# Performance work log

Measured on AMD Instinct MI355X. Metric: run time of the kernel, lower is better.

The kernel has to match this reference:

```python
import jax, jax.numpy as jnp
import numpy as np

BN_EPS = 1e-5


def _fps(xyz, n_centers):
    """Furthest point sampling. xyz: (B,N,3) -> idx (B,n_centers) int32.
    Deterministic start at index 0 (torch version uses randint start)."""
    B, N, _ = xyz.shape
    batch_ar = jnp.arange(B)

    def step(carry, _):
        distances, farthest = carry  # (B,N), (B,)
        center = xyz[batch_ar, farthest]  # (B,3)
        d = jnp.sum((xyz - center[:, None, :]) ** 2, axis=-1)  # (B,N)
        distances = jnp.minimum(distances, d)
        new_far = jnp.argmax(distances, axis=-1)
        return (distances, new_far), farthest

    init = (jnp.full((B, N), jnp.inf, dtype=xyz.dtype),
            jnp.zeros((B,), dtype=jnp.int32))
    _, idxs = jax.lax.scan(step, init, None, length=n_centers)  # (n_centers, B)
    return idxs.T  # (B, n_centers)


def _knn_group(xyz, centers, k):
    """xyz:(B,N,3), centers:(B,M,3) -> patches (B,M,k,3) center-relative."""
    # (B,M,N) squared distances
    dists = jnp.sum((centers[:, :, None, :] - xyz[:, None, :, :]) ** 2, axis=-1)
    _, idx = jax.lax.top_k(-dists, k)  # (B,M,k) smallest distances
    # gather neighbor coords: (B,M,k,3)
    patches = jnp.take_along_axis(xyz[:, None, :, :], idx[..., None], axis=2)
    return patches - centers[:, :, None, :]


def _bn_eval(x, gamma, beta):
    # BatchNorm1d in eval mode: running_mean=0, running_var=1
    return x * (gamma / jnp.sqrt(1.0 + BN_EPS)) + beta


def _mini_pointnet(patches, W1, b1, g1, bt1, W2, b2, g2, bt2, W3, b3, g3, bt3):
    B, M, k, C = patches.shape
    x = patches.reshape(B * M * k, C)
    x = jax.nn.relu(_bn_eval(x @ W1 + b1, g1, bt1))
    x = jax.nn.relu(_bn_eval(x @ W2 + b2, g2, bt2))
    x = jax.nn.relu(_bn_eval(x @ W3 + b3, g3, bt3))
    x = x.reshape(B * M, k, -1).max(axis=1)
    return x.reshape(B, M, -1)


def setup_inputs() -> dict:
    key = jax.random.key(0)
    ks = jax.random.split(key, 8)
    B, N = 16, 16384
    embed = 256

    def lin(kk, fan_in, fan_out):
        bound = 1.0 / np.sqrt(fan_in)
        k1, k2 = jax.random.split(kk)
        W = jax.random.uniform(k1, (fan_in, fan_out), jnp.float32, -bound, bound)
        b = jax.random.uniform(k2, (fan_out,), jnp.float32, -bound, bound)
        return W, b

    W1, b1 = lin(ks[1], 3, 64)
    W2, b2 = lin(ks[2], 64, 128)
    W3, b3 = lin(ks[3], 128, embed)
    return {
        "xyz": jax.random.normal(ks[0], (B, N, 3), jnp.float32),
        "W1": W1, "b1": b1, "g1": jnp.ones((64,)), "bt1": jnp.zeros((64,)),
        "W2": W2, "b2": b2, "g2": jnp.ones((128,)), "bt2": jnp.zeros((128,)),
        "W3": W3, "b3": b3, "g3": jnp.ones((embed,)), "bt3": jnp.zeros((embed,)),
        "n_centers": 256,
        "k": 32,
    }


def reference(xyz, W1, b1, g1, bt1, W2, b2, g2, bt2, W3, b3, g3, bt3,
              n_centers, k):
    center_idx = _fps(xyz, n_centers)  # (B, M)
    centers = jnp.take_along_axis(xyz, center_idx[..., None], axis=1)  # (B,M,3)
    patches = _knn_group(xyz, centers, k)  # (B,M,k,3)
    tokens = _mini_pointnet(patches, W1, b1, g1, bt1, W2, b2, g2, bt2,
                            W3, b3, g3, bt3)
    return tokens, centers
```

## Files before the change

kernel.cpp:

```cpp
#include <hip/hip_runtime.h>

constexpr int B   = 16;
constexpr int N   = 16384;
constexpr int M   = 256;
constexpr int K   = 32;
constexpr int EMB = 256;

__device__ __forceinline__ float sqdist(float px, float py, float pz,
                                        float cx, float cy, float cz) {
  float dx = __fsub_rn(px, cx);
  float dy = __fsub_rn(py, cy);
  float dz = __fsub_rn(pz, cz);
  return __fadd_rn(__fadd_rn(__fmul_rn(dx, dx), __fmul_rn(dy, dy)),
                   __fmul_rn(dz, dz));
}

constexpr int FT = 512;
constexpr int FP = N / FT;
constexpr int FW = FT / 64;

__global__ __launch_bounds__(FT, 2) void fps_kernel(
    const float* __restrict__ xyz, float* __restrict__ centers) {
  const int b = blockIdx.x;
  const int tid = threadIdx.x;
  const float* base = xyz + (size_t)b * N * 3;

  float px[FP], py[FP], pz[FP], dist[FP];
#pragma unroll
  for (int j = 0; j < FP; ++j) {
    int n = tid + j * FT;
    px[j] = base[n * 3 + 0];
    py[j] = base[n * 3 + 1];
    pz[j] = base[n * 3 + 2];
    dist[j] = __builtin_inff();
  }

  __shared__ float s_pv[2][FW];
  __shared__ int s_pn[2][FW];

  float cx = base[0], cy = base[1], cz = base[2];

  for (int it = 0; it < M; ++it) {
    if (tid == 0) {
      float* co = centers + ((size_t)b * M + it) * 3;
      co[0] = cx; co[1] = cy; co[2] = cz;
    }
    const int p = it & 1;

    float bv = -1.0f;
    int bj = 0;
#pragma unroll
    for (int j = 0; j < FP; ++j) {
      float d = sqdist(px[j], py[j], pz[j], cx, cy, cz);
      float nd = fminf(dist[j], d);
      dist[j] = nd;
      bool g = nd > bv;
      bv = g ? nd : bv;
      bj = g ? j : bj;
    }
    int bn = bj * FT + tid;

#pragma unroll
    for (int mm = 32; mm >= 1; mm >>= 1) {
      float ov = __shfl_xor(bv, mm, 64);
      int on = __shfl_xor(bn, mm, 64);
      if (ov > bv || (ov == bv && on < bn)) { bv = ov; bn = on; }
    }
    if ((tid & 63) == 0) {
      s_pv[p][tid >> 6] = bv;
      s_pn[p][tid >> 6] = bn;
    }
    __syncthreads();

    float v = s_pv[p][0];
    int n = s_pn[p][0];
#pragma unroll
    for (int w = 1; w < FW; ++w) {
      float ov = s_pv[p][w];
      int on = s_pn[p][w];
      if (ov > v || (ov == v && on < n)) { v = ov; n = on; }
    }
    cx = base[(size_t)n * 3 + 0];
    cy = base[(size_t)n * 3 + 1];
    cz = base[(size_t)n * 3 + 2];
  }
}

constexpr int KT = 256;
constexpr int CAP = 512;
constexpr int NBUCKET = 1024;

__global__ __launch_bounds__(KT) void knn_kernel(
    const float* __restrict__ xyz, const float* __restrict__ centers,
    float* __restrict__ patches) {
  const int blk = blockIdx.x;
  const int b = blk >> 8;
  const int tid = threadIdx.x;
  const float* base = xyz + (size_t)b * N * 3;

  __shared__ int hist[NBUCKET];
  __shared__ unsigned cb[CAP];
  __shared__ int ci[CAP];
  __shared__ int s_nin, s_ncand, s_tb;
  __shared__ int s_wsum[KT / 64];
  __shared__ float s_cc[3];

  if (tid == 0) {
    const float* c = centers + (size_t)blk * 3;
    s_cc[0] = c[0]; s_cc[1] = c[1]; s_cc[2] = c[2];
    s_nin = 0; s_ncand = 0;
  }
  for (int i = tid; i < NBUCKET; i += KT) hist[i] = 0;
  __syncthreads();

  const float cx = s_cc[0], cy = s_cc[1], cz = s_cc[2];

  for (int n = tid; n < N; n += KT) {
    float d = sqdist(base[n * 3], base[n * 3 + 1], base[n * 3 + 2], cx, cy, cz);
    atomicAdd(&hist[__float_as_uint(d) >> 21], 1);
  }
  __syncthreads();

  int h0[4];
  int loc = 0;
#pragma unroll
  for (int i = 0; i < 4; ++i) { h0[i] = hist[tid * 4 + i]; loc += h0[i]; }
  int lane = tid & 63, wid = tid >> 6;
  int scan = loc;
  for (int off = 1; off < 64; off <<= 1) {
    int o = __shfl_up(scan, off, 64);
    if (lane >= off) scan += o;
  }
  if (lane == 63) s_wsum[wid] = scan;
  __syncthreads();
  int woff = 0;
  for (int w = 0; w < wid; ++w) woff += s_wsum[w];
  int c0 = woff + scan - loc;
#pragma unroll
  for (int i = 0; i < 4; ++i) {
    int c1 = c0 + h0[i];
    if (c0 < K && c1 >= K) s_tb = tid * 4 + i;
    c0 = c1;
  }
  __syncthreads();
  const int tb = s_tb;
  const unsigned lo = (unsigned)tb << 21;
  const unsigned hi = (unsigned)(tb + 1) << 21;

  for (int n = tid; n < N; n += KT) {
    float x = base[n * 3], y = base[n * 3 + 1], z = base[n * 3 + 2];
    float d = sqdist(x, y, z, cx, cy, cz);
    unsigned bits = __float_as_uint(d);
    if (bits < lo) {
      int pos = atomicAdd(&s_nin, 1);
      float* p = patches + ((size_t)blk * K + pos) * 3;
      p[0] = __fsub_rn(x, cx); p[1] = __fsub_rn(y, cy); p[2] = __fsub_rn(z, cz);
    } else if (bits < hi) {
      int q = atomicAdd(&s_ncand, 1);
      if (q < CAP) { cb[q] = bits; ci[q] = n; }
    }
  }
  __syncthreads();

  const int nin = s_nin;
  const int ncand = min(s_ncand, CAP);
  const int nsel = K - nin;
  for (int j = tid; j < ncand; j += KT) {
    unsigned bj = cb[j];
    int ij = ci[j];
    int rank = 0;
    for (int i2 = 0; i2 < ncand; ++i2) {
      unsigned bv = cb[i2];
      int iv = ci[i2];
      rank += (bv < bj || (bv == bj && iv < ij)) ? 1 : 0;
    }
    if (rank < nsel) {
      float x = base[ij * 3], y = base[ij * 3 + 1], z = base[ij * 3 + 2];
      float* p = patches + ((size_t)blk * K + nin + rank) * 3;
      p[0] = __fsub_rn(x, cx); p[1] = __fsub_rn(y, cy); p[2] = __fsub_rn(z, cz);
    }
  }
}

constexpr int MT = 128;

__global__ __launch_bounds__(MT) void mlp_kernel(
    const float* __restrict__ patches,
    const float* __restrict__ W1, const float* __restrict__ b1,
    const float* __restrict__ g1, const float* __restrict__ bt1,
    const float* __restrict__ W2, const float* __restrict__ b2,
    const float* __restrict__ g2, const float* __restrict__ bt2,
    const float* __restrict__ W3, const float* __restrict__ b3,
    const float* __restrict__ g3, const float* __restrict__ bt3,
    float* __restrict__ tokens) {
  const int pm = blockIdx.x;
  const int tid = threadIdx.x;
  __shared__ float xs[3][K];
  __shared__ float h1s[64 * K];
  __shared__ float h2s[128 * K];
  __shared__ float pms[2][EMB];

  const float* patch = patches + (size_t)pm * (K * 3);
  if (tid < 96) xs[tid % 3][tid / 3] = patch[tid];
  __syncthreads();

  const int cg = tid & 63;
  const int half = tid >> 6;
  const int pt0 = half * 16;
  const float rs = 1.0f / sqrtf(1.0f + 1e-5f);

  {
    const int c = cg;
    const float w0 = W1[c], w1 = W1[64 + c], w2 = W1[128 + c];
    const float bb = b1[c];
    const float sc = g1[c] * rs, be = bt1[c];
    float o[16];
#pragma unroll
    for (int p = 0; p < 16; ++p) {
      int pt = pt0 + p;
      float a = xs[0][pt] * w0 + xs[1][pt] * w1 + xs[2][pt] * w2 + bb;
      o[p] = fmaxf(a * sc + be, 0.0f);
    }
    const int so = (c & 7) << 2;
#pragma unroll
    for (int p4 = 0; p4 < 16; p4 += 4) {
      *(float4*)&h1s[c * K + ((pt0 + p4) ^ so)] =
          make_float4(o[p4], o[p4 + 1], o[p4 + 2], o[p4 + 3]);
    }
  }
  __syncthreads();

  {
    const int c = cg * 2;
    float acc0[16], acc1[16];
    const float bb0 = b2[c], bb1 = b2[c + 1];
#pragma unroll
    for (int p = 0; p < 16; ++p) { acc0[p] = bb0; acc1[p] = bb1; }
    for (int k = 0; k < 64; ++k) {
      const float2 w = *(const float2*)(W2 + k * 128 + c);
      const int so = (k & 7) << 2;
      float4 x0 = *(const float4*)&h1s[k * K + ((pt0 + 0) ^ so)];
      float4 x1 = *(const float4*)&h1s[k * K + ((pt0 + 4) ^ so)];
      float4 x2 = *(const float4*)&h1s[k * K + ((pt0 + 8) ^ so)];
      float4 x3 = *(const float4*)&h1s[k * K + ((pt0 + 12) ^ so)];
      float xv[16] = {x0.x, x0.y, x0.z, x0.w, x1.x, x1.y, x1.z, x1.w,
                      x2.x, x2.y, x2.z, x2.w, x3.x, x3.y, x3.z, x3.w};
#pragma unroll
      for (int p = 0; p < 16; ++p) {
        acc0[p] += xv[p] * w.x;
        acc1[p] += xv[p] * w.y;
      }
    }
    const float sc0 = g2[c] * rs, be0 = bt2[c];
    const float sc1 = g2[c + 1] * rs, be1 = bt2[c + 1];
    float o0[16], o1[16];
#pragma unroll
    for (int p = 0; p < 16; ++p) {
      o0[p] = fmaxf(acc0[p] * sc0 + be0, 0.0f);
      o1[p] = fmaxf(acc1[p] * sc1 + be1, 0.0f);
    }
    const int soa = (c & 7) << 2, sob = ((c + 1) & 7) << 2;
#pragma unroll
    for (int p4 = 0; p4 < 16; p4 += 4) {
      *(float4*)&h2s[c * K + ((pt0 + p4) ^ soa)] =
          make_float4(o0[p4], o0[p4 + 1], o0[p4 + 2], o0[p4 + 3]);
      *(float4*)&h2s[(c + 1) * K + ((pt0 + p4) ^ sob)] =
          make_float4(o1[p4], o1[p4 + 1], o1[p4 + 2], o1[p4 + 3]);
    }
  }
  __syncthreads();

  {
    const int c = cg * 4;
    float acc[4][16];
#pragma unroll
    for (int i = 0; i < 4; ++i) {
      const float bb = b3[c + i];
#pragma unroll
      for (int p = 0; p < 16; ++p) acc[i][p] = bb;
    }
    for (int k = 0; k < 128; ++k) {
      const float4 w = *(const float4*)(W3 + (size_t)k * 256 + c);
      const int so = (k & 7) << 2;
      float4 x0 = *(const float4*)&h2s[k * K + ((pt0 + 0) ^ so)];
      float4 x1 = *(const float4*)&h2s[k * K + ((pt0 + 4) ^ so)];
      float4 x2 = *(const float4*)&h2s[k * K + ((pt0 + 8) ^ so)];
      float4 x3 = *(const float4*)&h2s[k * K + ((pt0 + 12) ^ so)];
      float xv[16] = {x0.x, x0.y, x0.z, x0.w, x1.x, x1.y, x1.z, x1.w,
                      x2.x, x2.y, x2.z, x2.w, x3.x, x3.y, x3.z, x3.w};
#pragma unroll
      for (int p = 0; p < 16; ++p) {
        acc[0][p] += xv[p] * w.x;
        acc[1][p] += xv[p] * w.y;
        acc[2][p] += xv[p] * w.z;
        acc[3][p] += xv[p] * w.w;
      }
    }
#pragma unroll
    for (int i = 0; i < 4; ++i) {
      const float sc = g3[c + i] * rs, be = bt3[c + i];
      float mx = 0.0f;
#pragma unroll
      for (int p = 0; p < 16; ++p)
        mx = fmaxf(mx, fmaxf(acc[i][p] * sc + be, 0.0f));
      pms[half][c + i] = mx;
    }
  }
  __syncthreads();

  {
    const int c2 = tid * 2;
    float* to = tokens + (size_t)pm * EMB;
    to[c2] = fmaxf(pms[0][c2], pms[1][c2]);
    to[c2 + 1] = fmaxf(pms[0][c2 + 1], pms[1][c2 + 1]);
  }
}

extern "C" void kernel_launch(void* const* d_in, const int* in_sizes, int n_in,
                              void* d_out, int out_size, void* d_ws,
                              size_t ws_size, hipStream_t stream) {
  const float* xyz = (const float*)d_in[0];
  const float* W1 = (const float*)d_in[1];
  const float* b1 = (const float*)d_in[2];
  const float* g1 = (const float*)d_in[3];
  const float* bt1 = (const float*)d_in[4];
  const float* W2 = (const float*)d_in[5];
  const float* b2 = (const float*)d_in[6];
  const float* g2 = (const float*)d_in[7];
  const float* bt2 = (const float*)d_in[8];
  const float* W3 = (const float*)d_in[9];
  const float* b3 = (const float*)d_in[10];
  const float* g3 = (const float*)d_in[11];
  const float* bt3 = (const float*)d_in[12];

  float* tokens = (float*)d_out;
  float* centers = tokens + (size_t)B * M * EMB;
  float* patches = (float*)d_ws;

  fps_kernel<<<B, FT, 0, stream>>>(xyz, centers);
  knn_kernel<<<B * M, KT, 0, stream>>>(xyz, centers, patches);
  mlp_kernel<<<B * M, MT, 0, stream>>>(patches, W1, b1, g1, bt1, W2, b2, g2,
                                       bt2, W3, b3, g3, bt3, tokens);
}
```

Baseline: 813.4 us.

## Split FPS across eight cooperating blocks per batch with global-memory handshakes

Furthest point sampling is spread over 8 workgroups per batch (128 blocks instead of 16). Each block handles 2048 points and publishes its local argmax and that point's coordinates to a global record with release/acquire atomics. Every block then spins until all peers have posted for the iteration and reduces the 8 candidates itself. This uses far more CUs for the sequential 256-iteration loop, at the cost of a cross-block spin barrier every iteration. It also relies on all 128 blocks being co-resident and on an extra init kernel that zeroes the sync records.

After: 1.466 ms. 80.3% more time.

```diff
diff --git a/kernel.cpp b/kernel.cpp
--- a/kernel.cpp
+++ b/kernel.cpp
@@ -15,50 +15,72 @@
                    __fmul_rn(dz, dz));
 }
 
-constexpr int FT = 512;
-constexpr int FP = N / FT;
-constexpr int FW = FT / 64;
-
-__global__ __launch_bounds__(FT, 2) void fps_kernel(
-    const float* __restrict__ xyz, float* __restrict__ centers) {
-  const int b = blockIdx.x;
+constexpr int FBLK = 8;
+constexpr int FTH  = 256;
+constexpr int FPTS = N / FBLK;
+constexpr int FPT  = FPTS / FTH;
+constexpr int RECI = 8;
+constexpr size_t PATCH_FLOATS = (size_t)B * M * K * 3;
+
+#define FPS_REP8(X) X(0) X(1) X(2) X(3) X(4) X(5) X(6) X(7)
+
+__global__ __launch_bounds__(256) void fps_init_kernel(int* __restrict__ sync) {
+  const int tot = B * FBLK * RECI;
+  for (int i = threadIdx.x; i < tot; i += 256) sync[i] = 0;
+}
+
+__global__ __launch_bounds__(FTH, 2) void fps_kernel(
+    const float* __restrict__ xyz, float* __restrict__ centers,
+    int* __restrict__ sync) {
+  const int gb = blockIdx.x;
+  const int b  = gb >> 3;
+  const int sb = gb & 7;
   const int tid = threadIdx.x;
   const float* base = xyz + (size_t)b * N * 3;
-
-  float px[FP], py[FP], pz[FP], dist[FP];
-#pragma unroll
-  for (int j = 0; j < FP; ++j) {
-    int n = tid + j * FT;
-    px[j] = base[n * 3 + 0];
-    py[j] = base[n * 3 + 1];
-    pz[j] = base[n * 3 + 2];
-    dist[j] = __builtin_inff();
-  }
-
-  __shared__ float s_pv[2][FW];
-  __shared__ int s_pn[2][FW];
+  const int pbase = sb * FPTS;
+  int* recs  = sync + (size_t)b * (FBLK * RECI);
+  int* myrec = recs + sb * RECI;
+
+#define FPS_DECL(i) float x##i, y##i, z##i, d##i;
+  FPS_REP8(FPS_DECL)
+#undef FPS_DECL
+#define FPS_LOAD(i) { const int n = pbase + tid + (i) * FTH; \
+    x##i = base[n * 3 + 0];                                   \
+    y##i = base[n * 3 + 1];                                   \
+    z##i = base[n * 3 + 2];                                   \
+    d##i = __builtin_inff(); }
+  FPS_REP8(FPS_LOAD)
+#undef FPS_LOAD
+
+  __shared__ float s_pv[FTH / 64];
+  __shared__ int s_pn[FTH / 64];
+  __shared__ float s_c[3];
 
   float cx = base[0], cy = base[1], cz = base[2];
 
   for (int it = 0; it < M; ++it) {
-    if (tid == 0) {
+    if (sb == 0 && tid == 0) {
       float* co = centers + ((size_t)b * M + it) * 3;
       co[0] = cx; co[1] = cy; co[2] = cz;
     }
-    const int p = it & 1;
 
     float bv = -1.0f;
     int bj = 0;
-#pragma unroll
-    for (int j = 0; j < FP; ++j) {
-      float d = sqdist(px[j], py[j], pz[j], cx, cy, cz);
-      float nd = fminf(dist[j], d);
-      dist[j] = nd;
-      bool g = nd > bv;
-      bv = g ? nd : bv;
-      bj = g ? j : bj;
-    }
-    int bn = bj * FT + tid;
+#define FPS_UPD(i) {                                          \
+    float ddx = __fsub_rn(x##i, cx);                          \
+    float ddy = __fsub_rn(y##i, cy);                          \
+    float ddz = __fsub_rn(z##i, cz);                          \
+    float dd = __fadd_rn(__fadd_rn(__fmul_rn(ddx, ddx),       \
+                                   __fmul_rn(ddy, ddy)),      \
+                         __fmul_rn(ddz, ddz));                \
+    float nd = fminf(d##i, dd);                               \
+    d##i = nd;                                                \
+    bool g = nd > bv;                                         \
+    bv = g ? nd : bv;                                         \
+    bj = g ? (i) : bj; }
+    FPS_REP8(FPS_UPD)
+#undef FPS_UPD
+    int bn = pbase + (bj << 8) + tid;
 
 #pragma unroll
     for (int mm = 32; mm >= 1; mm >>= 1) {
@@ -66,23 +88,69 @@
       int on = __shfl_xor(bn, mm, 64);
       if (ov > bv || (ov == bv && on < bn)) { bv = ov; bn = on; }
     }
-    if ((tid & 63) == 0) {
-      s_pv[p][tid >> 6] = bv;
-      s_pn[p][tid >> 6] = bn;
-    }
+    if ((tid & 63) == 0) { s_pv[tid >> 6] = bv; s_pn[tid >> 6] = bn; }
     __syncthreads();
 
-    float v = s_pv[p][0];
-    int n = s_pn[p][0];
-#pragma unroll
-    for (int w = 1; w < FW; ++w) {
-      float ov = s_pv[p][w];
-      int on = s_pn[p][w];
+    float v = s_pv[0];
+    int n = s_pn[0];
+#pragma unroll
+    for (int w = 1; w < FTH / 64; ++w) {
+      float ov = s_pv[w];
+      int on = s_pn[w];
       if (ov > v || (ov == v && on < n)) { v = ov; n = on; }
     }
-    cx = base[(size_t)n * 3 + 0];
-    cy = base[(size_t)n * 3 + 1];
-    cz = base[(size_t)n * 3 + 2];
+
+    const int loc = n - pbase;
+    if (tid == (loc & 255)) {
+      const int j = loc >> 8;
+      float wx = x0, wy = y0, wz = z0;
+      if (j == 1) { wx = x1; wy = y1; wz = z1; }
+      if (j == 2) { wx = x2; wy = y2; wz = z2; }
+      if (j == 3) { wx = x3; wy = y3; wz = z3; }
+      if (j == 4) { wx = x4; wy = y4; wz = z4; }
+      if (j == 5) { wx = x5; wy = y5; wz = z5; }
+      if (j == 6) { wx = x6; wy = y6; wz = z6; }
+      if (j == 7) { wx = x7; wy = y7; wz = z7; }
+      __hip_atomic_store(myrec + 0, __float_as_int(v), __ATOMIC_RELAXED,
+                         __HIP_MEMORY_SCOPE_AGENT);
+      __hip_atomic_store(myrec + 1, n, __ATOMIC_RELAXED,
+                         __HIP_MEMORY_SCOPE_AGENT);
+      __hip_atomic_store(myrec + 2, __float_as_int(wx), __ATOMIC_RELAXED,
+                         __HIP_MEMORY_SCOPE_AGENT);
+      __hip_atomic_store(myrec + 3, __float_as_int(wy), __ATOMIC_RELAXED,
+                         __HIP_MEMORY_SCOPE_AGENT);
+      __hip_atomic_store(myrec + 4, __float_as_int(wz), __ATOMIC_RELAXED,
+                         __HIP_MEMORY_SCOPE_AGENT);
+      __hip_atomic_store(myrec + 5, it + 1, __ATOMIC_RELEASE,
+                         __HIP_MEMORY_SCOPE_AGENT);
+    }
+
+    if (tid < FBLK) {
+      int* r = recs + tid * RECI;
+      while (__hip_atomic_load(r + 5, __ATOMIC_ACQUIRE,
+                               __HIP_MEMORY_SCOPE_AGENT) < it + 1) {}
+      float rv = __int_as_float(__hip_atomic_load(r + 0, __ATOMIC_RELAXED,
+                                                  __HIP_MEMORY_SCOPE_AGENT));
+      int rn = __hip_atomic_load(r + 1, __ATOMIC_RELAXED,
+                                 __HIP_MEMORY_SCOPE_AGENT);
+      float rcx = __int_as_float(__hip_atomic_load(r + 2, __ATOMIC_RELAXED,
+                                                   __HIP_MEMORY_SCOPE_AGENT));
+      float rcy = __int_as_float(__hip_atomic_load(r + 3, __ATOMIC_RELAXED,
+                                                   __HIP_MEMORY_SCOPE_AGENT));
+      float rcz = __int_as_float(__hip_atomic_load(r + 4, __ATOMIC_RELAXED,
+                                                   __HIP_MEMORY_SCOPE_AGENT));
+      float v2 = rv;
+      int n2 = rn;
+#pragma unroll
+      for (int m2 = 1; m2 <= 4; m2 <<= 1) {
+        float ov = __shfl_xor(v2, m2, 8);
+        int on = __shfl_xor(n2, m2, 8);
+        if (ov > v2 || (ov == v2 && on < n2)) { v2 = ov; n2 = on; }
+      }
+      if (rn == n2) { s_c[0] = rcx; s_c[1] = rcy; s_c[2] = rcz; }
+    }
+    __syncthreads();
+    cx = s_c[0]; cy = s_c[1]; cz = s_c[2];
   }
 }
 
@@ -336,8 +404,10 @@
   float* tokens = (float*)d_out;
   float* centers = tokens + (size_t)B * M * EMB;
   float* patches = (float*)d_ws;
-
-  fps_kernel<<<B, FT, 0, stream>>>(xyz, centers);
+  int* sync = (int*)((char*)d_ws + PATCH_FLOATS * sizeof(float));
+
+  fps_init_kernel<<<1, 256, 0, stream>>>(sync);
+  fps_kernel<<<B * FBLK, FTH, 0, stream>>>(xyz, centers, sync);
   knn_kernel<<<B * M, KT, 0, stream>>>(xyz, centers, patches);
   mlp_kernel<<<B * M, MT, 0, stream>>>(patches, W1, b1, g1, bt1, W2, b2, g2,
                                        bt2, W3, b3, g3, bt3, tokens);
```

## Restructure FPS to 1024 threads with LDS-resident points and distances

Applied to the files above, without the earlier changes.

The FPS kernel moves from 512 threads holding all points in registers to 1024 threads. The running distances now live in shared memory, 7 of 16 point slices are staged in LDS, and the other 9 are re-read from global memory every iteration. The goal is to cut register pressure and raise per-block parallelism for this serial-iteration kernel. The cost is LDS traffic every iteration, repeated global or L2 loads, and only one block per CU given the large shared footprint.

Measured after the change: 1.013 ms. +24.6%, slower.

```diff
diff --git a/kernel.cpp b/kernel.cpp
--- a/kernel.cpp
+++ b/kernel.cpp
@@ -15,30 +15,36 @@
                    __fmul_rn(dz, dz));
 }
 
-constexpr int FT = 512;
-constexpr int FP = N / FT;
+constexpr int FT = 1024;
+constexpr int LPT = 7;
+constexpr int SPT = 9;
 constexpr int FW = FT / 64;
 
-__global__ __launch_bounds__(FT, 2) void fps_kernel(
+__global__ __launch_bounds__(FT) void fps_kernel(
     const float* __restrict__ xyz, float* __restrict__ centers) {
   const int b = blockIdx.x;
   const int tid = threadIdx.x;
   const float* base = xyz + (size_t)b * N * 3;
 
-  float px[FP], py[FP], pz[FP], dist[FP];
-#pragma unroll
-  for (int j = 0; j < FP; ++j) {
-    int n = tid + j * FT;
-    px[j] = base[n * 3 + 0];
-    py[j] = base[n * 3 + 1];
-    pz[j] = base[n * 3 + 2];
-    dist[j] = __builtin_inff();
-  }
-
+  __shared__ float s_dist[N];
+  __shared__ float s_cx[LPT * FT];
+  __shared__ float s_cy[LPT * FT];
+  __shared__ float s_cz[LPT * FT];
   __shared__ float s_pv[2][FW];
   __shared__ int s_pn[2][FW];
 
+#pragma unroll
+  for (int i = 0; i < LPT; ++i) {
+    const int n = i * FT + tid;
+    s_cx[n] = base[n * 3 + 0];
+    s_cy[n] = base[n * 3 + 1];
+    s_cz[n] = base[n * 3 + 2];
+  }
+#pragma unroll
+  for (int i = 0; i < 16; ++i) s_dist[i * FT + tid] = __builtin_inff();
+
   float cx = base[0], cy = base[1], cz = base[2];
+  __syncthreads();
 
   for (int it = 0; it < M; ++it) {
     if (tid == 0) {
@@ -49,16 +55,39 @@
 
     float bv = -1.0f;
     int bj = 0;
-#pragma unroll
-    for (int j = 0; j < FP; ++j) {
-      float d = sqdist(px[j], py[j], pz[j], cx, cy, cz);
-      float nd = fminf(dist[j], d);
-      dist[j] = nd;
+
+    float gx[SPT], gy[SPT], gz[SPT];
+#pragma unroll
+    for (int i = 0; i < SPT; ++i) {
+      const int n = (LPT + i) * FT + tid;
+      gx[i] = base[n * 3 + 0];
+      gy[i] = base[n * 3 + 1];
+      gz[i] = base[n * 3 + 2];
+    }
+
+#pragma unroll
+    for (int i = 0; i < LPT; ++i) {
+      const int n = i * FT + tid;
+      float d = sqdist(s_cx[n], s_cy[n], s_cz[n], cx, cy, cz);
+      float od = s_dist[n];
+      float nd = fminf(od, d);
+      s_dist[n] = nd;
       bool g = nd > bv;
       bv = g ? nd : bv;
-      bj = g ? j : bj;
-    }
-    int bn = bj * FT + tid;
+      bj = g ? i : bj;
+    }
+#pragma unroll
+    for (int i = 0; i < SPT; ++i) {
+      const int n = (LPT + i) * FT + tid;
+      float d = sqdist(gx[i], gy[i], gz[i], cx, cy, cz);
+      float od = s_dist[n];
+      float nd = fminf(od, d);
+      s_dist[n] = nd;
+      bool g = nd > bv;
+      bv = g ? nd : bv;
+      bj = g ? (LPT + i) : bj;
+    }
+    int bn = (bj << 10) + tid;
 
 #pragma unroll
     for (int mm = 32; mm >= 1; mm >>= 1) {
@@ -66,10 +95,7 @@
       int on = __shfl_xor(bn, mm, 64);
       if (ov > bv || (ov == bv && on < bn)) { bv = ov; bn = on; }
     }
-    if ((tid & 63) == 0) {
-      s_pv[p][tid >> 6] = bv;
-      s_pn[p][tid >> 6] = bn;
-    }
+    if ((tid & 63) == 0) { s_pv[p][tid >> 6] = bv; s_pn[p][tid >> 6] = bn; }
     __syncthreads();
 
     float v = s_pv[p][0];
```
